# Kernel tuning notes

Hardware: AMD Instinct MI355X
Metric: run time of the kernel (lower is better)

The kernel has to match this reference:

```python
import jax, jax.numpy as jnp
import numpy as np

MICRO_BATCHES = 4
NUM_EXPERTS = 8  # world_size=1 -> num_local_experts = 8
EPS = 1e-5


def setup_inputs() -> dict:
    key = jax.random.key(0)
    ks = jax.random.split(key, 8)
    B, S, D = 8, 2048, 1024
    E, F = NUM_EXPERTS, 4 * D
    x = jax.random.normal(ks[0], (B, S, D), dtype=jnp.float32)
    gamma = jnp.ones((D,), jnp.float32)
    beta = jnp.zeros((D,), jnp.float32)
    gate_w = jax.random.normal(ks[1], (E, D), jnp.float32) * (1.0 / np.sqrt(D))
    w1 = jax.random.normal(ks[2], (E, D, F), jnp.float32) * (1.0 / np.sqrt(D))
    b1 = jnp.zeros((E, F), jnp.float32)
    w2 = jax.random.normal(ks[3], (E, F, D), jnp.float32) * (1.0 / np.sqrt(F))
    b2 = jnp.zeros((E, D), jnp.float32)
    return {"x": x, "gamma": gamma, "beta": beta, "gate_w": gate_w,
            "w1": w1, "b1": b1, "w2": w2, "b2": b2}


def reference(x, gamma, beta, gate_w, w1, b1, w2, b2):
    B, S, D = x.shape
    E = w1.shape[0]
    # micro-batch chunking along batch dim (chunk(MICRO_BATCHES, dim=0))
    xf = x.reshape(MICRO_BATCHES, -1, D)            # [MB, T, D], T = B/MB * S
    T = xf.shape[1]
    # residual (gated_input) is the pre-LN flat input
    # moe_norm: LayerNorm over last dim, biased variance, eps=1e-5
    mu = jnp.mean(xf, axis=-1, keepdims=True)
    var = jnp.mean(jnp.square(xf - mu), axis=-1, keepdims=True)
    xn = (xf - mu) * jax.lax.rsqrt(var + EPS) * gamma + beta  # [MB, T, D]
    # gate logits + topk are computed in the source but discarded
    _logits = jnp.einsum('mtd,ed->mte', xn, gate_w)
    _ = jax.lax.top_k(_logits, 2)
    # dispatch/combine are identity for world_size=1; tokens split round-robin
    # into num_local_experts contiguous chunks per micro-batch
    tpe = T // E
    xe = xn.reshape(MICRO_BATCHES, E, tpe, D)       # [MB, E, tpe, D]
    h = jax.nn.gelu(jnp.einsum('metd,edf->metf', xe, w1) + b1[None, :, None, :],
                    approximate=False)
    y = jnp.einsum('metf,efd->metd', h, w2) + b2[None, :, None, :]
    out = xf + y.reshape(MICRO_BATCHES, T, D)       # residual add
    return out.reshape(B, S, D)
```

## Files before the change

kernel.cpp:

```cpp
#include <hip/hip_runtime.h>
#include <stdint.h>
#include <math.h>

typedef unsigned short ushort_t;
typedef __attribute__((ext_vector_type(8))) short bf16x8;
typedef __attribute__((ext_vector_type(4))) float f32x4;

#define SLOT 32768
#define EPI_STRIDE 1032

#define DS_READ(D, B, O) asm volatile("ds_read_b128 %0, %1 offset:" O : "=v"(D) : "v"(B))
#define SCHED0 __builtin_amdgcn_sched_barrier(0)
#define BAR __builtin_amdgcn_s_barrier()
#define WAITL0 asm volatile("s_waitcnt lgkmcnt(0)" ::: "memory")

__device__ __forceinline__ ushort_t f2bf(float f) {
  union { float f; unsigned u; } cv; cv.f = f;
  unsigned r = cv.u + 0x7fffu + ((cv.u >> 16) & 1u);
  return (ushort_t)(r >> 16);
}

__device__ __forceinline__ void gl_lds16(const void* g, void* l) {
  typedef __attribute__((address_space(1))) const char gchar;
  typedef __attribute__((address_space(3))) char lchar;
  __builtin_amdgcn_global_load_lds((gchar*)g, (lchar*)l, 16, 0, 0);
}

__device__ __forceinline__ unsigned lds_addr(void* p) {
  typedef __attribute__((address_space(3))) char lchar;
  return (unsigned)(unsigned long long)(lchar*)p;
}

__device__ __forceinline__ f32x4 MFMA(bf16x8 a, bf16x8 b, f32x4 c) {
  return __builtin_amdgcn_mfma_f32_16x16x32_bf16(a, b, c, 0, 0, 0);
}

__global__ __launch_bounds__(256) void ln_kernel(const float* __restrict__ x,
                                                 const float* __restrict__ gamma,
                                                 const float* __restrict__ beta,
                                                 ushort_t* __restrict__ xn) {
  const int row = blockIdx.x;
  const int t = threadIdx.x;
  const float4 v = ((const float4*)(x + (size_t)row * 1024))[t];
  float s  = v.x + v.y + v.z + v.w;
  float ss = v.x * v.x + v.y * v.y + v.z * v.z + v.w * v.w;
#pragma unroll
  for (int o = 32; o >= 1; o >>= 1) {
    s  += __shfl_xor(s, o);
    ss += __shfl_xor(ss, o);
  }
  __shared__ float red[10];
  const int wave = t >> 6, lane = t & 63;
  if (lane == 0) { red[wave] = s; red[4 + wave] = ss; }
  __syncthreads();
  if (t == 0) {
    float S  = red[0] + red[1] + red[2] + red[3];
    float SS = red[4] + red[5] + red[6] + red[7];
    float mu  = S * (1.0f / 1024.0f);
    float var = SS * (1.0f / 1024.0f) - mu * mu;
    red[8] = mu;
    red[9] = rsqrtf(var + 1e-5f);
  }
  __syncthreads();
  const float mu = red[8], rs = red[9];
  const float4 g = ((const float4*)gamma)[t];
  const float4 b = ((const float4*)beta)[t];
  ushort4 o;
  o.x = f2bf((v.x - mu) * rs * g.x + b.x);
  o.y = f2bf((v.y - mu) * rs * g.y + b.y);
  o.z = f2bf((v.z - mu) * rs * g.z + b.z);
  o.w = f2bf((v.w - mu) * rs * g.w + b.w);
  ((ushort4*)(xn + (size_t)row * 1024))[t] = o;
}

__global__ __launch_bounds__(256) void transpose_cast(const float* __restrict__ in,
                                                      ushort_t* __restrict__ out,
                                                      int R, int C) {
  __shared__ float tile[32][33];
  const int e = blockIdx.z;
  const float* src = in + (size_t)e * R * C;
  ushort_t* dst = out + (size_t)e * R * C;
  const int c0 = blockIdx.x * 32, r0 = blockIdx.y * 32;
  const int tx = threadIdx.x, ty = threadIdx.y;
#pragma unroll
  for (int j = 0; j < 32; j += 8)
    tile[ty + j][tx] = src[(size_t)(r0 + ty + j) * C + c0 + tx];
  __syncthreads();
#pragma unroll
  for (int j = 0; j < 32; j += 8)
    dst[(size_t)(c0 + ty + j) * R + r0 + tx] = f2bf(tile[tx][ty + j]);
}


__device__ __forceinline__ void stage_half(const ushort_t* gsrc, int lda,
                                           char* half_base, int kt, int tid) {
  const int rr = tid >> 2;
  const int gs = (tid & 3) ^ ((tid >> 3) & 3);
  gl_lds16(gsrc + (size_t)rr * lda + kt + gs * 8, half_base + (tid >> 6) * 1024);
}

template <int BASE>
__device__ __forceinline__ void mfma16(const bf16x8& a0, const bf16x8& a1,
                                       const bf16x8& a2, const bf16x8& a3,
                                       const bf16x8& b0, const bf16x8& b1,
                                       const bf16x8& b2, const bf16x8& b3,
                                       f32x4 (&acc)[8][4]) {
  __builtin_amdgcn_s_setprio(1);
  acc[BASE+0][0] = MFMA(a0, b0, acc[BASE+0][0]);
  acc[BASE+0][1] = MFMA(a0, b1, acc[BASE+0][1]);
  acc[BASE+0][2] = MFMA(a0, b2, acc[BASE+0][2]);
  acc[BASE+0][3] = MFMA(a0, b3, acc[BASE+0][3]);
  acc[BASE+1][0] = MFMA(a1, b0, acc[BASE+1][0]);
  acc[BASE+1][1] = MFMA(a1, b1, acc[BASE+1][1]);
  acc[BASE+1][2] = MFMA(a1, b2, acc[BASE+1][2]);
  acc[BASE+1][3] = MFMA(a1, b3, acc[BASE+1][3]);
  acc[BASE+2][0] = MFMA(a2, b0, acc[BASE+2][0]);
  acc[BASE+2][1] = MFMA(a2, b1, acc[BASE+2][1]);
  acc[BASE+2][2] = MFMA(a2, b2, acc[BASE+2][2]);
  acc[BASE+2][3] = MFMA(a2, b3, acc[BASE+2][3]);
  acc[BASE+3][0] = MFMA(a3, b0, acc[BASE+3][0]);
  acc[BASE+3][1] = MFMA(a3, b1, acc[BASE+3][1]);
  acc[BASE+3][2] = MFMA(a3, b2, acc[BASE+3][2]);
  acc[BASE+3][3] = MFMA(a3, b3, acc[BASE+3][3]);
  __builtin_amdgcn_s_setprio(0);
}

template <int SIDX, int VM, bool STG>
__device__ __forceinline__ void slot_body(unsigned aBase, unsigned bBase, char* smem,
                                          int kt3, const ushort_t* gA, const ushort_t* gB,
                                          int lda, int tid, f32x4 (&acc)[8][4]) {
  const unsigned sA = aBase + SIDX * SLOT;
  const unsigned sB = bBase + SIDX * SLOT;
  char* nstg = smem + ((SIDX + 3) & 3) * SLOT;
  bf16x8 a0, a1, a2, a3, b0, b1, b2, b3;
  DS_READ(b0, sB, "0");    DS_READ(b1, sB, "1024");
  DS_READ(b2, sB, "2048"); DS_READ(b3, sB, "3072");
  DS_READ(a0, sA, "0");    DS_READ(a1, sA, "1024");
  DS_READ(a2, sA, "2048"); DS_READ(a3, sA, "3072");
  if (STG) {
    stage_half(gA, lda, nstg, kt3, tid);
    stage_half(gA + (size_t)128 * lda, lda, nstg + 8192, kt3, tid);
  }
  SCHED0;
  BAR;
  WAITL0;
  SCHED0;
  mfma16<0>(a0, a1, a2, a3, b0, b1, b2, b3, acc);
  SCHED0;
  if (VM == 6)      asm volatile("s_waitcnt vmcnt(6)" ::: "memory");
  else if (VM == 4) asm volatile("s_waitcnt vmcnt(4)" ::: "memory");
  else if (VM == 0) asm volatile("s_waitcnt vmcnt(0)" ::: "memory");
  BAR;
  SCHED0;
  DS_READ(a0, sA, "4096"); DS_READ(a1, sA, "5120");
  DS_READ(a2, sA, "6144"); DS_READ(a3, sA, "7168");
  if (STG) {
    stage_half(gB, lda, nstg + 16384, kt3, tid);
    stage_half(gB + (size_t)128 * lda, lda, nstg + 24576, kt3, tid);
  }
  SCHED0;
  BAR;
  WAITL0;
  SCHED0;
  mfma16<4>(a0, a1, a2, a3, b0, b1, b2, b3, acc);
  SCHED0;
  BAR;
  SCHED0;
}

template <int EPI, int LDA, int LDC, int KTOT>
__global__ __launch_bounds__(512, 2) void gemm256(const ushort_t* __restrict__ A,
                                                  const ushort_t* __restrict__ Bw,
                                                  const float* __restrict__ bias,
                                                  const float* __restrict__ resid,
                                                  ushort_t* __restrict__ Hout,
                                                  float* __restrict__ Fout) {
  extern __shared__ char smem[];
  const int tid = threadIdx.x;
  const int wave = tid >> 6, lane = tid & 63;

  const int bid = blockIdx.x;
  const int c = bid & 7, l = bid >> 3;
  const int tm = c * 8 + (l & 7);
  const int tn = l >> 3;
  const int row0 = tm * 256;
  const int col0 = tn * 256;
  const int e = (row0 >> 9) & 7;

  const ushort_t* gA = A + (size_t)row0 * LDA;
  const ushort_t* gB = Bw + ((size_t)e * LDC + col0) * LDA;

  const int NT = KTOT / 32;

  const int wm = wave >> 2, wn = wave & 3;
  const int l15 = lane & 15, g = lane >> 4;
  const int sw = ((g ^ ((lane >> 1) & 3)) << 4);
  const int a_off = wm * 8192 + l15 * 64 + sw;
  const int b_off = 16384 + (wn >> 1) * 8192 + (wn & 1) * 4096 + l15 * 64 + sw;

  const unsigned aBase = lds_addr(smem) + a_off;
  const unsigned bBase = lds_addr(smem) + b_off;

  f32x4 acc[8][4] = {};

#pragma unroll
  for (int T = 0; T < 3; ++T) {
    char* s = smem + T * SLOT;
    stage_half(gA, LDA, s, T * 32, tid);
    stage_half(gA + (size_t)128 * LDA, LDA, s + 8192, T * 32, tid);
    stage_half(gB, LDA, s + 16384, T * 32, tid);
    stage_half(gB + (size_t)128 * LDA, LDA, s + 24576, T * 32, tid);
  }
  asm volatile("s_waitcnt vmcnt(8)" ::: "memory");
  BAR;
  SCHED0;

  for (int T = 0; T < NT - 4; T += 4) {
    slot_body<0, 6, true>(aBase, bBase, smem, (T + 3) * 32, gA, gB, LDA, tid, acc);
    slot_body<1, 6, true>(aBase, bBase, smem, (T + 4) * 32, gA, gB, LDA, tid, acc);
    slot_body<2, 6, true>(aBase, bBase, smem, (T + 5) * 32, gA, gB, LDA, tid, acc);
    slot_body<3, 6, true>(aBase, bBase, smem, (T + 6) * 32, gA, gB, LDA, tid, acc);
  }
  slot_body<0, 6, true >(aBase, bBase, smem, (NT - 1) * 32, gA, gB, LDA, tid, acc);
  slot_body<1, 4, false>(aBase, bBase, smem, 0,             gA, gB, LDA, tid, acc);
  slot_body<2, 0, false>(aBase, bBase, smem, 0,             gA, gB, LDA, tid, acc);
  slot_body<3, -1, false>(aBase, bBase, smem, 0,            gA, gB, LDA, tid, acc);

  __syncthreads();

  float bv[4];
#pragma unroll
  for (int ni = 0; ni < 4; ni++)
    bv[ni] = bias[e * LDC + col0 + wn * 64 + ni * 16 + l15];

#pragma unroll
  for (int r = 0; r < 4; ++r) {
#pragma unroll
    for (int mh = 0; mh < 2; ++mh) {
      const int mi = 2 * r + mh;
      const int lrow = wm * 32 + mh * 16 + g * 4;
#pragma unroll
      for (int ni = 0; ni < 4; ++ni) {
        const int colb = (wn * 64 + ni * 16 + l15) * 4;
#pragma unroll
        for (int rr = 0; rr < 4; ++rr) {
          float v = acc[mi][ni][rr] + bv[ni];
          if (EPI == 0) {
            float v2 = v * v;
            float cc = fmaf(0.044715f, v2, 1.0f);
            float u  = exp2f(-2.3022078f * v * cc);
            v = __fdividef(v, 1.0f + u);
          }
          *(float*)(smem + (size_t)(lrow + rr) * EPI_STRIDE + colb) = v;
        }
      }
    }
    __syncthreads();
#pragma unroll
    for (int i = 0; i < 8; ++i) {
      const int chunk = i * 512 + tid;
      const int lr = chunk >> 6;
      const int cb = (chunk & 63) * 16;
      const float4 v4 = *(const float4*)(smem + (size_t)lr * EPI_STRIDE + cb);
      const int grow = row0 + (lr < 32 ? r * 32 + lr : 128 + r * 32 + (lr - 32));
      const int gcol = col0 + (chunk & 63) * 4;
      if (EPI == 0) {
        ushort4 o;
        o.x = f2bf(v4.x); o.y = f2bf(v4.y); o.z = f2bf(v4.z); o.w = f2bf(v4.w);
        *(ushort4*)(&Hout[(size_t)grow * LDC + gcol]) = o;
      } else {
        const float4 rs = *(const float4*)(&resid[(size_t)grow * LDC + gcol]);
        float4 o;
        o.x = v4.x + rs.x; o.y = v4.y + rs.y; o.z = v4.z + rs.z; o.w = v4.w + rs.w;
        *(float4*)(&Fout[(size_t)grow * LDC + gcol]) = o;
      }
    }
    __syncthreads();
  }
}

extern "C" void kernel_launch(void* const* d_in, const int* in_sizes, int n_in,
                              void* d_out, int out_size, void* d_ws, size_t ws_size,
                              hipStream_t stream) {
  const float* x     = (const float*)d_in[0];
  const float* gamma = (const float*)d_in[1];
  const float* beta  = (const float*)d_in[2];
  const float* w1    = (const float*)d_in[4];
  const float* b1    = (const float*)d_in[5];
  const float* w2    = (const float*)d_in[6];
  const float* b2    = (const float*)d_in[7];
  float* out = (float*)d_out;

  char* ws = (char*)d_ws;
  ushort_t* xn  = (ushort_t*)ws;
  ushort_t* w1t = (ushort_t*)(ws + 33554432);
  ushort_t* w2t = (ushort_t*)(ws + 33554432 + 67108864);
  ushort_t* h   = (ushort_t*)(ws + 33554432 + 2 * 67108864);

  hipFuncSetAttribute(reinterpret_cast<const void*>(&gemm256<0, 1024, 4096, 1024>),
                      hipFuncAttributeMaxDynamicSharedMemorySize, 131072);
  hipFuncSetAttribute(reinterpret_cast<const void*>(&gemm256<1, 4096, 1024, 4096>),
                      hipFuncAttributeMaxDynamicSharedMemorySize, 131072);

  ln_kernel<<<16384, 256, 0, stream>>>(x, gamma, beta, xn);
  transpose_cast<<<dim3(128, 32, 8), dim3(32, 8), 0, stream>>>(w1, w1t, 1024, 4096);
  transpose_cast<<<dim3(32, 128, 8), dim3(32, 8), 0, stream>>>(w2, w2t, 4096, 1024);

  gemm256<0, 1024, 4096, 1024><<<dim3(1024), 512, 131072, stream>>>(xn, w1t, b1, nullptr, h, nullptr);
  gemm256<1, 4096, 1024, 4096><<<dim3(256), 512, 131072, stream>>>(h, w2t, b2, x, nullptr, out);
}
```

Before: 425.3 us.

## Shrink GEMM tiles to 256x128 with 4 waves and double-buffered LDS

Both expert GEMMs now use 256x128 tiles computed by 256-thread blocks, in place of 256x256 tiles on 512-thread blocks. The 4-slot LDS pipeline with 3-deep prefetch becomes a 2-buffer ping-pong that needs one barrier per k-step, which cuts LDS use from 128KB to 48KB and doubles the grid size. The aim is more resident blocks and better load balance across CUs, fewer barriers, and better tail behaviour. The cost is less data reuse per tile, more global traffic for A, and a shallower prefetch that may expose memory latency (vmcnt(0) each step).

```diff
diff --git a/kernel.cpp b/kernel.cpp
--- a/kernel.cpp
+++ b/kernel.cpp
@@ -6,8 +6,8 @@
 typedef __attribute__((ext_vector_type(8))) short bf16x8;
 typedef __attribute__((ext_vector_type(4))) float f32x4;
 
-#define SLOT 32768
-#define EPI_STRIDE 1032
+#define SLOT 24576
+#define EPI_STRIDE 520
 
 #define DS_READ(D, B, O) asm volatile("ds_read_b128 %0, %1 offset:" O : "=v"(D) : "v"(B))
 #define SCHED0 __builtin_amdgcn_sched_barrier(0)
@@ -91,13 +91,6 @@
     dst[(size_t)(c0 + ty + j) * R + r0 + tx] = f2bf(tile[tx][ty + j]);
 }
 
-
-__device__ __forceinline__ void stage_half(const ushort_t* gsrc, int lda,
-                                           char* half_base, int kt, int tid) {
-  const int rr = tid >> 2;
-  const int gs = (tid & 3) ^ ((tid >> 3) & 3);
-  gl_lds16(gsrc + (size_t)rr * lda + kt + gs * 8, half_base + (tid >> 6) * 1024);
-}
 
 template <int BASE>
 __device__ __forceinline__ void mfma16(const bf16x8& a0, const bf16x8& a1,
@@ -125,56 +118,52 @@
   __builtin_amdgcn_s_setprio(0);
 }
 
-template <int SIDX, int VM, bool STG>
+template <int BUF, bool STG, int LDA>
 __device__ __forceinline__ void slot_body(unsigned aBase, unsigned bBase, char* smem,
-                                          int kt3, const ushort_t* gA, const ushort_t* gB,
-                                          int lda, int tid, f32x4 (&acc)[8][4]) {
-  const unsigned sA = aBase + SIDX * SLOT;
-  const unsigned sB = bBase + SIDX * SLOT;
-  char* nstg = smem + ((SIDX + 3) & 3) * SLOT;
+                                          const ushort_t* gA, const ushort_t* gB,
+                                          size_t sOff, int kt, int tid,
+                                          f32x4 (&acc)[8][4]) {
+  const unsigned sA = aBase + BUF * SLOT;
+  const unsigned sB = bBase + BUF * SLOT;
+  char* nb = smem + (BUF ^ 1) * SLOT;
+  const int wdst = (tid >> 6) * 1024;
   bf16x8 a0, a1, a2, a3, b0, b1, b2, b3;
   DS_READ(b0, sB, "0");    DS_READ(b1, sB, "1024");
   DS_READ(b2, sB, "2048"); DS_READ(b3, sB, "3072");
   DS_READ(a0, sA, "0");    DS_READ(a1, sA, "1024");
   DS_READ(a2, sA, "2048"); DS_READ(a3, sA, "3072");
   if (STG) {
-    stage_half(gA, lda, nstg, kt3, tid);
-    stage_half(gA + (size_t)128 * lda, lda, nstg + 8192, kt3, tid);
-  }
-  SCHED0;
-  BAR;
+    gl_lds16(gA + sOff + kt,                     nb + wdst);
+    gl_lds16(gA + (size_t)64  * LDA + sOff + kt, nb + 4096  + wdst);
+    gl_lds16(gA + (size_t)128 * LDA + sOff + kt, nb + 8192  + wdst);
+    gl_lds16(gA + (size_t)192 * LDA + sOff + kt, nb + 12288 + wdst);
+    gl_lds16(gB + sOff + kt,                     nb + 16384 + wdst);
+    gl_lds16(gB + (size_t)64  * LDA + sOff + kt, nb + 20480 + wdst);
+  }
+  SCHED0;
   WAITL0;
   SCHED0;
   mfma16<0>(a0, a1, a2, a3, b0, b1, b2, b3, acc);
-  SCHED0;
-  if (VM == 6)      asm volatile("s_waitcnt vmcnt(6)" ::: "memory");
-  else if (VM == 4) asm volatile("s_waitcnt vmcnt(4)" ::: "memory");
-  else if (VM == 0) asm volatile("s_waitcnt vmcnt(0)" ::: "memory");
-  BAR;
   SCHED0;
   DS_READ(a0, sA, "4096"); DS_READ(a1, sA, "5120");
   DS_READ(a2, sA, "6144"); DS_READ(a3, sA, "7168");
-  if (STG) {
-    stage_half(gB, lda, nstg + 16384, kt3, tid);
-    stage_half(gB + (size_t)128 * lda, lda, nstg + 24576, kt3, tid);
-  }
-  SCHED0;
+  SCHED0;
+  WAITL0;
+  SCHED0;
+  mfma16<4>(a0, a1, a2, a3, b0, b1, b2, b3, acc);
+  SCHED0;
+  if (STG) asm volatile("s_waitcnt vmcnt(0)" ::: "memory");
   BAR;
-  WAITL0;
-  SCHED0;
-  mfma16<4>(a0, a1, a2, a3, b0, b1, b2, b3, acc);
-  SCHED0;
-  BAR;
   SCHED0;
 }
 
 template <int EPI, int LDA, int LDC, int KTOT>
-__global__ __launch_bounds__(512, 2) void gemm256(const ushort_t* __restrict__ A,
-                                                  const ushort_t* __restrict__ Bw,
-                                                  const float* __restrict__ bias,
-                                                  const float* __restrict__ resid,
-                                                  ushort_t* __restrict__ Hout,
-                                                  float* __restrict__ Fout) {
+__global__ __launch_bounds__(256, 2) void gemmk(const ushort_t* __restrict__ A,
+                                                const ushort_t* __restrict__ Bw,
+                                                const float* __restrict__ bias,
+                                                const float* __restrict__ resid,
+                                                ushort_t* __restrict__ Hout,
+                                                float* __restrict__ Fout) {
   extern __shared__ char smem[];
   const int tid = threadIdx.x;
   const int wave = tid >> 6, lane = tid & 63;
@@ -184,47 +173,48 @@
   const int tm = c * 8 + (l & 7);
   const int tn = l >> 3;
   const int row0 = tm * 256;
-  const int col0 = tn * 256;
-  const int e = (row0 >> 9) & 7;
+  const int col0 = tn * 128;
+  const int e = (tm >> 1) & 7;
 
   const ushort_t* gA = A + (size_t)row0 * LDA;
   const ushort_t* gB = Bw + ((size_t)e * LDC + col0) * LDA;
 
   const int NT = KTOT / 32;
 
-  const int wm = wave >> 2, wn = wave & 3;
+  const int wm = wave >> 1, wn = wave & 1;
   const int l15 = lane & 15, g = lane >> 4;
   const int sw = ((g ^ ((lane >> 1) & 3)) << 4);
   const int a_off = wm * 8192 + l15 * 64 + sw;
-  const int b_off = 16384 + (wn >> 1) * 8192 + (wn & 1) * 4096 + l15 * 64 + sw;
-
+  const int b_off = 16384 + (wn * 64 + l15) * 64 + sw;
   const unsigned aBase = lds_addr(smem) + a_off;
   const unsigned bBase = lds_addr(smem) + b_off;
 
+  const int gs = (tid & 3) ^ ((tid >> 3) & 3);
+  const size_t sOff = (size_t)(tid >> 2) * LDA + gs * 8;
+
   f32x4 acc[8][4] = {};
 
-#pragma unroll
-  for (int T = 0; T < 3; ++T) {
-    char* s = smem + T * SLOT;
-    stage_half(gA, LDA, s, T * 32, tid);
-    stage_half(gA + (size_t)128 * LDA, LDA, s + 8192, T * 32, tid);
-    stage_half(gB, LDA, s + 16384, T * 32, tid);
-    stage_half(gB + (size_t)128 * LDA, LDA, s + 24576, T * 32, tid);
-  }
-  asm volatile("s_waitcnt vmcnt(8)" ::: "memory");
+  {
+    char* nb = smem;
+    const int wdst = (tid >> 6) * 1024;
+    gl_lds16(gA + sOff,                     nb + wdst);
+    gl_lds16(gA + (size_t)64  * LDA + sOff, nb + 4096  + wdst);
+    gl_lds16(gA + (size_t)128 * LDA + sOff, nb + 8192  + wdst);
+    gl_lds16(gA + (size_t)192 * LDA + sOff, nb + 12288 + wdst);
+    gl_lds16(gB + sOff,                     nb + 16384 + wdst);
+    gl_lds16(gB + (size_t)64  * LDA + sOff, nb + 20480 + wdst);
+  }
+  asm volatile("s_waitcnt vmcnt(0)" ::: "memory");
   BAR;
   SCHED0;
 
-  for (int T = 0; T < NT - 4; T += 4) {
-    slot_body<0, 6, true>(aBase, bBase, smem, (T + 3) * 32, gA, gB, LDA, tid, acc);
-    slot_body<1, 6, true>(aBase, bBase, smem, (T + 4) * 32, gA, gB, LDA, tid, acc);
-    slot_body<2, 6, true>(aBase, bBase, smem, (T + 5) * 32, gA, gB, LDA, tid, acc);
-    slot_body<3, 6, true>(aBase, bBase, smem, (T + 6) * 32, gA, gB, LDA, tid, acc);
-  }
-  slot_body<0, 6, true >(aBase, bBase, smem, (NT - 1) * 32, gA, gB, LDA, tid, acc);
-  slot_body<1, 4, false>(aBase, bBase, smem, 0,             gA, gB, LDA, tid, acc);
-  slot_body<2, 0, false>(aBase, bBase, smem, 0,             gA, gB, LDA, tid, acc);
-  slot_body<3, -1, false>(aBase, bBase, smem, 0,            gA, gB, LDA, tid, acc);
+#pragma unroll 1
+  for (int T = 0; T + 2 < NT; T += 2) {
+    slot_body<0, true, LDA>(aBase, bBase, smem, gA, gB, sOff, (T + 1) * 32, tid, acc);
+    slot_body<1, true, LDA>(aBase, bBase, smem, gA, gB, sOff, (T + 2) * 32, tid, acc);
+  }
+  slot_body<0, true,  LDA>(aBase, bBase, smem, gA, gB, sOff, (NT - 1) * 32, tid, acc);
+  slot_body<1, false, LDA>(aBase, bBase, smem, gA, gB, sOff, 0, tid, acc);
 
   __syncthreads();
 
@@ -258,12 +248,12 @@
     __syncthreads();
 #pragma unroll
     for (int i = 0; i < 8; ++i) {
-      const int chunk = i * 512 + tid;
-      const int lr = chunk >> 6;
-      const int cb = (chunk & 63) * 16;
+      const int chunk = i * 256 + tid;
+      const int lr = chunk >> 5;
+      const int cb = (chunk & 31) * 16;
       const float4 v4 = *(const float4*)(smem + (size_t)lr * EPI_STRIDE + cb);
       const int grow = row0 + (lr < 32 ? r * 32 + lr : 128 + r * 32 + (lr - 32));
-      const int gcol = col0 + (chunk & 63) * 4;
+      const int gcol = col0 + (chunk & 31) * 4;
       if (EPI == 0) {
         ushort4 o;
         o.x = f2bf(v4.x); o.y = f2bf(v4.y); o.z = f2bf(v4.z); o.w = f2bf(v4.w);
@@ -297,15 +287,15 @@
   ushort_t* w2t = (ushort_t*)(ws + 33554432 + 67108864);
   ushort_t* h   = (ushort_t*)(ws + 33554432 + 2 * 67108864);
 
-  hipFuncSetAttribute(reinterpret_cast<const void*>(&gemm256<0, 1024, 4096, 1024>),
-                      hipFuncAttributeMaxDynamicSharedMemorySize, 131072);
-  hipFuncSetAttribute(reinterpret_cast<const void*>(&gemm256<1, 4096, 1024, 4096>),
-                      hipFuncAttributeMaxDynamicSharedMemorySize, 131072);
+  hipFuncSetAttribute(reinterpret_cast<const void*>(&gemmk<0, 1024, 4096, 1024>),
+                      hipFuncAttributeMaxDynamicSharedMemorySize, 49152);
+  hipFuncSetAttribute(reinterpret_cast<const void*>(&gemmk<1, 4096, 1024, 4096>),
+                      hipFuncAttributeMaxDynamicSharedMemorySize, 49152);
 
   ln_kernel<<<16384, 256, 0, stream>>>(x, gamma, beta, xn);
   transpose_cast<<<dim3(128, 32, 8), dim3(32, 8), 0, stream>>>(w1, w1t, 1024, 4096);
   transpose_cast<<<dim3(32, 128, 8), dim3(32, 8), 0, stream>>>(w2, w2t, 4096, 1024);
 
-  gemm256<0, 1024, 4096, 1024><<<dim3(1024), 512, 131072, stream>>>(xn, w1t, b1, nullptr, h, nullptr);
-  gemm256<1, 4096, 1024, 4096><<<dim3(256), 512, 131072, stream>>>(h, w2t, b2, x, nullptr, out);
-}
+  gemmk<0, 1024, 4096, 1024><<<dim3(2048), 256, 49152, stream>>>(xn, w1t, b1, nullptr, h, nullptr);
+  gemmk<1, 4096, 1024, 4096><<<dim3(512), 256, 49152, stream>>>(h, w2t, b2, x, nullptr, out);
+}
```

Result: no change. 433.1 us (+1.8%).
